# Kernel tuning notes

Measured on AMD Instinct MI355X. Metric: run time of the kernel, lower is better.

The kernel has to match this reference:

```python
import jax, jax.numpy as jnp
import numpy as np
import math

EMBED = 1024
HEADS = 16
HEAD_DIM = EMBED // HEADS
B, S = 2, 2048


def setup_inputs() -> dict:
    key = jax.random.key(0)
    ks = jax.random.split(key, 11)
    s = 1.0 / math.sqrt(EMBED)
    return {
        "query": jax.random.normal(ks[0], (B, S, EMBED), jnp.float32),
        "key_": jax.random.normal(ks[1], (B, S, EMBED), jnp.float32),
        "value": jax.random.normal(ks[2], (B, S, EMBED), jnp.float32),
        "Wq": jax.random.normal(ks[3], (EMBED, EMBED), jnp.float32) * s,
        "bq": jax.random.normal(ks[4], (EMBED,), jnp.float32) * s,
        "Wk": jax.random.normal(ks[5], (EMBED, EMBED), jnp.float32) * s,
        "bk": jax.random.normal(ks[6], (EMBED,), jnp.float32) * s,
        "Wv": jax.random.normal(ks[7], (EMBED, EMBED), jnp.float32) * s,
        "bv": jax.random.normal(ks[8], (EMBED,), jnp.float32) * s,
        "Wo": jax.random.normal(ks[9], (EMBED, EMBED), jnp.float32) * s,
        "bo": jax.random.normal(ks[10], (EMBED,), jnp.float32) * s,
    }


def reference(query, key_, value, Wq, bq, Wk, bk, Wv, bv, Wo, bo):
    b, s, e = query.shape
    # projections (torch Linear: x @ W.T + b)
    q = query @ Wq.T + bq
    k = key_ @ Wk.T + bk
    v = value @ Wv.T + bv
    # [B, H, S, hd]
    q = q.reshape(b, s, HEADS, HEAD_DIM).transpose(0, 2, 1, 3)
    k = k.reshape(b, s, HEADS, HEAD_DIM).transpose(0, 2, 1, 3)
    v = v.reshape(b, s, HEADS, HEAD_DIM).transpose(0, 2, 1, 3)
    scores = jnp.einsum("bhqd,bhkd->bhqk", q, k) / math.sqrt(HEAD_DIM)
    attn = jax.nn.softmax(scores, axis=-1)
    out = jnp.einsum("bhqk,bhkd->bhqd", attn, v)
    out = out.transpose(0, 2, 1, 3).reshape(b, s, e)
    return out @ Wo.T + bo
```

## Files before the change

kernel.cpp:

```cpp
#include <hip/hip_runtime.h>
#include <hip/hip_bf16.h>

using bf16_t = __bf16;
using bf16x4 = __attribute__((ext_vector_type(4))) __bf16;
using bf16x8 = __attribute__((ext_vector_type(8))) __bf16;
using f32x4  = __attribute__((ext_vector_type(4))) float;
using u32 = unsigned int;

constexpr int S_ = 2048, E_ = 1024, M_ = 4096;
constexpr size_t MAT_A = (size_t)M_ * E_;
constexpr size_t MAT_W = (size_t)E_ * E_;

__device__ __forceinline__ bf16_t tobf(float f) {
  unsigned u = __builtin_bit_cast(unsigned, f);
  unsigned short r = (unsigned short)((u + 0x7fffu + ((u >> 16) & 1u)) >> 16);
  return __builtin_bit_cast(bf16_t, r);
}
__device__ __forceinline__ u32 packbf2(float a, float b) {
  u32 ua = __builtin_bit_cast(u32, a) + 0x8000u;
  u32 ub = __builtin_bit_cast(u32, b) + 0x8000u;
  return (ua >> 16) | (ub & 0xffff0000u);
}
__device__ __forceinline__ void async_lds16(const bf16_t* g, bf16_t* l) {
  __builtin_amdgcn_global_load_lds(
      (const __attribute__((address_space(1))) unsigned int*)g,
      (__attribute__((address_space(3))) unsigned int*)l, 16, 0, 0);
}

__global__ __launch_bounds__(256) void cvt7(
    const float* __restrict__ s0, const float* __restrict__ s1,
    const float* __restrict__ s2, const float* __restrict__ s3,
    const float* __restrict__ s4, const float* __restrict__ s5,
    const float* __restrict__ s6,
    bf16_t* __restrict__ d0, bf16_t* __restrict__ d1,
    bf16_t* __restrict__ d2, bf16_t* __restrict__ d3,
    bf16_t* __restrict__ d4, bf16_t* __restrict__ d5,
    bf16_t* __restrict__ d6) {
  const int w = blockIdx.y;
  const size_t n = w < 3 ? MAT_A : MAT_W;
  size_t i = ((size_t)blockIdx.x * 256 + threadIdx.x) * 8;
  if (i >= n) return;
  const float* s = w == 0 ? s0 : w == 1 ? s1 : w == 2 ? s2 : w == 3 ? s3
                 : w == 4 ? s4 : w == 5 ? s5 : s6;
  bf16_t* d = w == 0 ? d0 : w == 1 ? d1 : w == 2 ? d2 : w == 3 ? d3
            : w == 4 ? d4 : w == 5 ? d5 : d6;
  float4 a = *(const float4*)(s + i);
  float4 b = *(const float4*)(s + i + 4);
  bf16x8 o;
  o[0] = tobf(a.x); o[1] = tobf(a.y); o[2] = tobf(a.z); o[3] = tobf(a.w);
  o[4] = tobf(b.x); o[5] = tobf(b.y); o[6] = tobf(b.z); o[7] = tobf(b.w);
  *(bf16x8*)(d + i) = o;
}

__global__ __launch_bounds__(256) void gemm_qkv(
    const bf16_t* __restrict__ xq, const bf16_t* __restrict__ xk,
    const bf16_t* __restrict__ xv, const bf16_t* __restrict__ wq,
    const bf16_t* __restrict__ wk, const bf16_t* __restrict__ wv,
    const float* __restrict__ bq, const float* __restrict__ bk,
    const float* __restrict__ bv, bf16_t* __restrict__ outb,
    bf16_t* __restrict__ Vt) {
  constexpr int K = 1024, N = 1024, BK = 32;
  constexpr float SC = 0.18033688011f;
  __shared__ __align__(16) bf16_t As[128 * BK];
  __shared__ __align__(16) bf16_t Bs[128 * BK];
  const int which = blockIdx.y >> 3;
  const bf16_t* X = which == 0 ? xq : which == 1 ? xk : xv;
  const bf16_t* W = which == 0 ? wq : which == 1 ? wk : wv;
  const float* bias = which == 0 ? bq : which == 1 ? bk : bv;
  const int row0 = blockIdx.x * 128, col0 = (blockIdx.y & 7) * 128;

  const int tid = threadIdx.x, lane = tid & 63, wave = tid >> 6;
  const int l15 = lane & 15, q = lane >> 4;
  const int wm = (wave & 1) * 64, wn = (wave >> 1) * 64;
  const f32x4 fzero = {0.f, 0.f, 0.f, 0.f};

  f32x4 acc[4][4];
#pragma unroll
  for (int i = 0; i < 4; ++i)
#pragma unroll
    for (int j = 0; j < 4; ++j) acc[i][j] = fzero;

  const bf16_t* gA = X + (size_t)(row0 + wave * 32 + (lane >> 2)) * K + (lane & 3) * 8;
  const bf16_t* gB = W + (size_t)(col0 + wave * 32 + (lane >> 2)) * K + (lane & 3) * 8;
  bf16_t* lA = As + wave * 32 * BK;
  bf16_t* lB = Bs + wave * 32 * BK;

  for (int k0 = 0; k0 < K; k0 += BK) {
    __syncthreads();
    async_lds16(gA + k0, lA);
    async_lds16(gA + k0 + 16 * K, lA + 16 * BK);
    async_lds16(gB + k0, lB);
    async_lds16(gB + k0 + 16 * K, lB + 16 * BK);
    __syncthreads();
    bf16x8 af[4], bw[4];
#pragma unroll
    for (int i = 0; i < 4; ++i)
      af[i] = *(const bf16x8*)(As + (wm + i * 16 + l15) * BK + q * 8);
#pragma unroll
    for (int j = 0; j < 4; ++j)
      bw[j] = *(const bf16x8*)(Bs + (wn + j * 16 + l15) * BK + q * 8);
#pragma unroll
    for (int i = 0; i < 4; ++i)
#pragma unroll
      for (int j = 0; j < 4; ++j)
        acc[i][j] = __builtin_amdgcn_mfma_f32_16x16x32_bf16(af[i], bw[j],
                                                            acc[i][j], 0, 0, 0);
  }

  if (which < 2) {
    const float sc = which == 0 ? SC : 1.0f;
    bf16_t* C = outb + (size_t)which * MAT_A;
#pragma unroll
    for (int j = 0; j < 4; ++j) {
      const int col = col0 + wn + j * 16 + l15;
      const float bc = bias[col];
#pragma unroll
      for (int i = 0; i < 4; ++i)
#pragma unroll
        for (int r = 0; r < 4; ++r) {
          const int row = row0 + wm + i * 16 + q * 4 + r;
          C[(size_t)row * N + col] = tobf((acc[i][j][r] + bc) * sc);
        }
    }
  } else {
#pragma unroll
    for (int j = 0; j < 4; ++j) {
      const int col = col0 + wn + j * 16 + l15;
      const float bc = bias[col];
      const int head = col >> 6, d = col & 63;
#pragma unroll
      for (int i = 0; i < 4; ++i) {
        const int row = row0 + wm + i * 16 + q * 4;
        const int bb = row >> 11, tok = row & 2047;
        bf16x4 o;
#pragma unroll
        for (int r = 0; r < 4; ++r) o[r] = tobf(acc[i][j][r] + bc);
        *(bf16x4*)(Vt + ((size_t)(bb * 16 + head) * 64 + d) * S_ + tok) = o;
      }
    }
  }
}

__global__ __launch_bounds__(256) void gemm_o(const bf16_t* __restrict__ X,
                                              const bf16_t* __restrict__ W,
                                              const float* __restrict__ bias,
                                              float* __restrict__ C) {
  constexpr int K = 1024, N = 1024, BK = 32;
  __shared__ __align__(16) bf16_t As[64 * BK];
  __shared__ __align__(16) bf16_t Bs[128 * BK];
  const int tid = threadIdx.x, lane = tid & 63, wave = tid >> 6;
  const int l15 = lane & 15, q = lane >> 4;
  const int row0 = blockIdx.x * 64, col0 = blockIdx.y * 128;
  const int wm = (wave & 1) * 32, wn = (wave >> 1) * 64;
  const f32x4 fzero = {0.f, 0.f, 0.f, 0.f};

  f32x4 acc[2][4];
#pragma unroll
  for (int i = 0; i < 2; ++i)
#pragma unroll
    for (int j = 0; j < 4; ++j) acc[i][j] = fzero;

  const bf16_t* gA = X + (size_t)(row0 + wave * 16 + (lane >> 2)) * K + (lane & 3) * 8;
  const bf16_t* gB = W + (size_t)(col0 + wave * 32 + (lane >> 2)) * K + (lane & 3) * 8;
  bf16_t* lA = As + wave * 16 * BK;
  bf16_t* lB = Bs + wave * 32 * BK;

  for (int k0 = 0; k0 < K; k0 += BK) {
    __syncthreads();
    async_lds16(gA + k0, lA);
    async_lds16(gB + k0, lB);
    async_lds16(gB + k0 + 16 * K, lB + 16 * BK);
    __syncthreads();
    bf16x8 af[2], bw[4];
#pragma unroll
    for (int i = 0; i < 2; ++i)
      af[i] = *(const bf16x8*)(As + (wm + i * 16 + l15) * BK + q * 8);
#pragma unroll
    for (int j = 0; j < 4; ++j)
      bw[j] = *(const bf16x8*)(Bs + (wn + j * 16 + l15) * BK + q * 8);
#pragma unroll
    for (int i = 0; i < 2; ++i)
#pragma unroll
      for (int j = 0; j < 4; ++j)
        acc[i][j] = __builtin_amdgcn_mfma_f32_16x16x32_bf16(af[i], bw[j],
                                                            acc[i][j], 0, 0, 0);
  }

#pragma unroll
  for (int j = 0; j < 4; ++j) {
    const int col = col0 + wn + j * 16 + l15;
    const float bc = bias[col];
#pragma unroll
    for (int i = 0; i < 2; ++i)
#pragma unroll
      for (int r = 0; r < 4; ++r) {
        const int row = row0 + wm + i * 16 + q * 4 + r;
        C[(size_t)row * N + col] = acc[i][j][r] + bc;
      }
  }
}

__global__ __launch_bounds__(256) void attn_mfma(
    const bf16_t* __restrict__ Qm, const bf16_t* __restrict__ Km,
    const bf16_t* __restrict__ Vtg, bf16_t* __restrict__ Om) {
  constexpr int LDP = 72;
  __shared__ __align__(16) bf16_t Ks[2][64 * 64];
  __shared__ __align__(16) bf16_t Vs[2][64 * 64];
  __shared__ __align__(16) bf16_t Ps[4][2][16 * LDP];

  const int tid = threadIdx.x, lane = tid & 63, wave = tid >> 6;
  const int l15 = lane & 15, q = lane >> 4;
  const int bh = blockIdx.x & 31, qb = blockIdx.x >> 5;
  const int b = bh >> 4, h = bh & 15;
  const size_t rowbase = (size_t)b * S_;
  const int hcol = h * 64;
  const int q0 = qb * 128 + wave * 32;

  const int srow = lane >> 3;
  const int schunk = (lane & 7) ^ srow;
  const bf16_t* gK = Km + (rowbase + wave * 16 + srow) * E_ + hcol + schunk * 8;
  const bf16_t* gV = Vtg + ((size_t)bh * 64 + wave * 16 + srow) * S_ + schunk * 8;

  bf16x8 qf[2][2];
#pragma unroll
  for (int qt = 0; qt < 2; ++qt) {
    const bf16_t* qp = Qm + (rowbase + q0 + qt * 16 + l15) * E_ + hcol + q * 8;
    qf[qt][0] = *(const bf16x8*)qp;
    qf[qt][1] = *(const bf16x8*)(qp + 32);
  }

  const f32x4 fzero = {0.f, 0.f, 0.f, 0.f};
  f32x4 oacc[2][4];
#pragma unroll
  for (int qt = 0; qt < 2; ++qt)
#pragma unroll
    for (int mt = 0; mt < 4; ++mt) oacc[qt][mt] = fzero;
  float lsum[2] = {0.f, 0.f};

  const int rbase = l15 * 64;
  int ck[2];
  ck[0] = ((q) ^ (l15 & 7)) * 8;
  ck[1] = ((4 + q) ^ (l15 & 7)) * 8;
  bf16_t* pw0 = Ps[wave][0] + l15 * LDP;
  bf16_t* pw1 = Ps[wave][1] + l15 * LDP;

  async_lds16(gK, Ks[0] + wave * 1024);
  async_lds16(gK + (size_t)8 * E_, Ks[0] + wave * 1024 + 512);
  async_lds16(gV, Vs[0] + wave * 1024);
  async_lds16(gV + (size_t)8 * S_, Vs[0] + wave * 1024 + 512);

  for (int t = 0; t < 32; ++t) {
    const int pb = t & 1;
    __syncthreads();
    if (t + 1 < 32) {
      const size_t koff = (size_t)((t + 1) * 64) * E_;
      const int voff = (t + 1) * 64;
      bf16_t* dK = Ks[pb ^ 1] + wave * 1024;
      bf16_t* dV = Vs[pb ^ 1] + wave * 1024;
      async_lds16(gK + koff, dK);
      async_lds16(gK + koff + (size_t)8 * E_, dK + 512);
      async_lds16(gV + voff, dV);
      async_lds16(gV + voff + (size_t)8 * S_, dV + 512);
    }
    const bf16_t* Kbuf = Ks[pb];
    const bf16_t* Vbuf = Vs[pb];

#pragma unroll
    for (int nt = 0; nt < 4; ++nt) {
      bf16x8 a0 = *(const bf16x8*)(Kbuf + nt * 1024 + rbase + ck[0]);
      bf16x8 a1 = *(const bf16x8*)(Kbuf + nt * 1024 + rbase + ck[1]);
#pragma unroll
      for (int qt = 0; qt < 2; ++qt) {
        f32x4 st = fzero;
        st = __builtin_amdgcn_mfma_f32_16x16x32_bf16(a0, qf[qt][0], st, 0, 0, 0);
        st = __builtin_amdgcn_mfma_f32_16x16x32_bf16(a1, qf[qt][1], st, 0, 0, 0);
        float p0 = __builtin_amdgcn_exp2f(st[0]);
        float p1 = __builtin_amdgcn_exp2f(st[1]);
        float p2 = __builtin_amdgcn_exp2f(st[2]);
        float p3 = __builtin_amdgcn_exp2f(st[3]);
        lsum[qt] += (p0 + p1) + (p2 + p3);
        uint2 pk;
        pk.x = packbf2(p0, p1);
        pk.y = packbf2(p2, p3);
        *(uint2*)((qt ? pw1 : pw0) + nt * 16 + q * 4) = pk;
      }
    }

#pragma unroll
    for (int kk = 0; kk < 2; ++kk) {
      bf16x8 bp0 = *(const bf16x8*)(pw0 + kk * 32 + q * 8);
      bf16x8 bp1 = *(const bf16x8*)(pw1 + kk * 32 + q * 8);
#pragma unroll
      for (int mt = 0; mt < 4; ++mt) {
        bf16x8 av = *(const bf16x8*)(Vbuf + mt * 1024 + rbase + ck[kk]);
        oacc[0][mt] = __builtin_amdgcn_mfma_f32_16x16x32_bf16(av, bp0,
                                                              oacc[0][mt], 0, 0, 0);
        oacc[1][mt] = __builtin_amdgcn_mfma_f32_16x16x32_bf16(av, bp1,
                                                              oacc[1][mt], 0, 0, 0);
      }
    }
  }

#pragma unroll
  for (int qt = 0; qt < 2; ++qt) {
    float l = lsum[qt];
    l += __shfl_xor(l, 16);
    l += __shfl_xor(l, 32);
    const float inv = 1.0f / l;
    const size_t orow = (rowbase + q0 + qt * 16 + l15) * E_ + hcol + q * 4;
#pragma unroll
    for (int mt = 0; mt < 4; ++mt) {
      bf16x4 o;
#pragma unroll
      for (int r = 0; r < 4; ++r) o[r] = tobf(oacc[qt][mt][r] * inv);
      *(bf16x4*)(Om + orow + mt * 16) = o;
    }
  }
}

extern "C" void kernel_launch(void* const* d_in, const int* in_sizes, int n_in,
                              void* d_out, int out_size, void* d_ws, size_t ws_size,
                              hipStream_t stream) {
  const float* query = (const float*)d_in[0];
  const float* key_  = (const float*)d_in[1];
  const float* value = (const float*)d_in[2];
  const float* Wq = (const float*)d_in[3];
  const float* bq = (const float*)d_in[4];
  const float* Wk = (const float*)d_in[5];
  const float* bk = (const float*)d_in[6];
  const float* Wv = (const float*)d_in[7];
  const float* bv = (const float*)d_in[8];
  const float* Wo = (const float*)d_in[9];
  const float* bo = (const float*)d_in[10];

  bf16_t* qc  = (bf16_t*)d_ws;
  bf16_t* kc  = qc + MAT_A;
  bf16_t* vc  = kc + MAT_A;
  bf16_t* wqb = vc + MAT_A;
  bf16_t* wkb = wqb + MAT_W;
  bf16_t* wvb = wkb + MAT_W;
  bf16_t* wob = wvb + MAT_W;
  bf16_t* Qb  = wob + MAT_W;
  bf16_t* Kb  = Qb + MAT_A;
  bf16_t* Vt  = Kb + MAT_A;
  bf16_t* AOb = Vt + MAT_A;

  cvt7<<<dim3(MAT_A / 2048, 7), 256, 0, stream>>>(
      query, key_, value, Wq, Wk, Wv, Wo,
      qc, kc, vc, wqb, wkb, wvb, wob);
  gemm_qkv<<<dim3(32, 24), 256, 0, stream>>>(qc, kc, vc, wqb, wkb, wvb,
                                             bq, bk, bv, Qb, Vt);
  attn_mfma<<<512, 256, 0, stream>>>(Qb, Kb, Vt, AOb);
  gemm_o<<<dim3(64, 8), 256, 0, stream>>>(AOb, wob, bo, (float*)d_out);
}
```

Before: 238.9 us.

## Load K/V fragments directly from global and compute row sums via MFMA

Removes the LDS double-buffered async staging of K and V tiles and the per-iteration block barrier, so each wave loads its MFMA operand fragments straight from global memory (relying on L1/L2 for reuse across waves). The softmax denominator is now computed with an extra MFMA against a ones vector on the bf16-rounded probabilities, instead of scalar adds plus cross-lane shuffles. The cost is four times more global/L2 traffic for K and V per block, and load latency exposed without explicit prefetch.

```diff
diff --git a/kernel.cpp b/kernel.cpp
--- a/kernel.cpp
+++ b/kernel.cpp
@@ -204,8 +204,6 @@
     const bf16_t* __restrict__ Qm, const bf16_t* __restrict__ Km,
     const bf16_t* __restrict__ Vtg, bf16_t* __restrict__ Om) {
   constexpr int LDP = 72;
-  __shared__ __align__(16) bf16_t Ks[2][64 * 64];
-  __shared__ __align__(16) bf16_t Vs[2][64 * 64];
   __shared__ __align__(16) bf16_t Ps[4][2][16 * LDP];
 
   const int tid = threadIdx.x, lane = tid & 63, wave = tid >> 6;
@@ -216,11 +214,6 @@
   const int hcol = h * 64;
   const int q0 = qb * 128 + wave * 32;
 
-  const int srow = lane >> 3;
-  const int schunk = (lane & 7) ^ srow;
-  const bf16_t* gK = Km + (rowbase + wave * 16 + srow) * E_ + hcol + schunk * 8;
-  const bf16_t* gV = Vtg + ((size_t)bh * 64 + wave * 16 + srow) * S_ + schunk * 8;
-
   bf16x8 qf[2][2];
 #pragma unroll
   for (int qt = 0; qt < 2; ++qt) {
@@ -229,56 +222,44 @@
     qf[qt][1] = *(const bf16x8*)(qp + 32);
   }
 
+  bf16x8 onesv;
+#pragma unroll
+  for (int j = 0; j < 8; ++j)
+    onesv[j] = __builtin_bit_cast(bf16_t, (unsigned short)0x3F80);
+
   const f32x4 fzero = {0.f, 0.f, 0.f, 0.f};
   f32x4 oacc[2][4];
 #pragma unroll
   for (int qt = 0; qt < 2; ++qt)
 #pragma unroll
     for (int mt = 0; mt < 4; ++mt) oacc[qt][mt] = fzero;
-  float lsum[2] = {0.f, 0.f};
-
-  const int rbase = l15 * 64;
-  int ck[2];
-  ck[0] = ((q) ^ (l15 & 7)) * 8;
-  ck[1] = ((4 + q) ^ (l15 & 7)) * 8;
+  f32x4 lsacc[2] = {fzero, fzero};
+
+  const bf16_t* Kb = Km + (rowbase + l15) * E_ + hcol + q * 8;
+  const bf16_t* Vb = Vtg + ((size_t)bh * 64 + l15) * S_ + q * 8;
   bf16_t* pw0 = Ps[wave][0] + l15 * LDP;
   bf16_t* pw1 = Ps[wave][1] + l15 * LDP;
 
-  async_lds16(gK, Ks[0] + wave * 1024);
-  async_lds16(gK + (size_t)8 * E_, Ks[0] + wave * 1024 + 512);
-  async_lds16(gV, Vs[0] + wave * 1024);
-  async_lds16(gV + (size_t)8 * S_, Vs[0] + wave * 1024 + 512);
-
-  for (int t = 0; t < 32; ++t) {
-    const int pb = t & 1;
-    __syncthreads();
-    if (t + 1 < 32) {
-      const size_t koff = (size_t)((t + 1) * 64) * E_;
-      const int voff = (t + 1) * 64;
-      bf16_t* dK = Ks[pb ^ 1] + wave * 1024;
-      bf16_t* dV = Vs[pb ^ 1] + wave * 1024;
-      async_lds16(gK + koff, dK);
-      async_lds16(gK + koff + (size_t)8 * E_, dK + 512);
-      async_lds16(gV + voff, dV);
-      async_lds16(gV + voff + (size_t)8 * S_, dV + 512);
-    }
-    const bf16_t* Kbuf = Ks[pb];
-    const bf16_t* Vbuf = Vs[pb];
-
+  for (int kt = 0; kt < S_; kt += 64) {
+    bf16x8 kf[4][2];
 #pragma unroll
     for (int nt = 0; nt < 4; ++nt) {
-      bf16x8 a0 = *(const bf16x8*)(Kbuf + nt * 1024 + rbase + ck[0]);
-      bf16x8 a1 = *(const bf16x8*)(Kbuf + nt * 1024 + rbase + ck[1]);
+      const bf16_t* kp = Kb + (size_t)(kt + nt * 16) * E_;
+      kf[nt][0] = *(const bf16x8*)kp;
+      kf[nt][1] = *(const bf16x8*)(kp + 32);
+    }
+
+#pragma unroll
+    for (int nt = 0; nt < 4; ++nt) {
 #pragma unroll
       for (int qt = 0; qt < 2; ++qt) {
         f32x4 st = fzero;
-        st = __builtin_amdgcn_mfma_f32_16x16x32_bf16(a0, qf[qt][0], st, 0, 0, 0);
-        st = __builtin_amdgcn_mfma_f32_16x16x32_bf16(a1, qf[qt][1], st, 0, 0, 0);
+        st = __builtin_amdgcn_mfma_f32_16x16x32_bf16(kf[nt][0], qf[qt][0], st, 0, 0, 0);
+        st = __builtin_amdgcn_mfma_f32_16x16x32_bf16(kf[nt][1], qf[qt][1], st, 0, 0, 0);
         float p0 = __builtin_amdgcn_exp2f(st[0]);
         float p1 = __builtin_amdgcn_exp2f(st[1]);
         float p2 = __builtin_amdgcn_exp2f(st[2]);
         float p3 = __builtin_amdgcn_exp2f(st[3]);
-        lsum[qt] += (p0 + p1) + (p2 + p3);
         uint2 pk;
         pk.x = packbf2(p0, p1);
         pk.y = packbf2(p2, p3);
@@ -290,9 +271,11 @@
     for (int kk = 0; kk < 2; ++kk) {
       bf16x8 bp0 = *(const bf16x8*)(pw0 + kk * 32 + q * 8);
       bf16x8 bp1 = *(const bf16x8*)(pw1 + kk * 32 + q * 8);
+      lsacc[0] = __builtin_amdgcn_mfma_f32_16x16x32_bf16(onesv, bp0, lsacc[0], 0, 0, 0);
+      lsacc[1] = __builtin_amdgcn_mfma_f32_16x16x32_bf16(onesv, bp1, lsacc[1], 0, 0, 0);
 #pragma unroll
       for (int mt = 0; mt < 4; ++mt) {
-        bf16x8 av = *(const bf16x8*)(Vbuf + mt * 1024 + rbase + ck[kk]);
+        bf16x8 av = *(const bf16x8*)(Vb + (size_t)(mt * 16) * S_ + kt + kk * 32);
         oacc[0][mt] = __builtin_amdgcn_mfma_f32_16x16x32_bf16(av, bp0,
                                                               oacc[0][mt], 0, 0, 0);
         oacc[1][mt] = __builtin_amdgcn_mfma_f32_16x16x32_bf16(av, bp1,
@@ -303,10 +286,7 @@
 
 #pragma unroll
   for (int qt = 0; qt < 2; ++qt) {
-    float l = lsum[qt];
-    l += __shfl_xor(l, 16);
-    l += __shfl_xor(l, 32);
-    const float inv = 1.0f / l;
+    const float inv = 1.0f / lsacc[qt][0];
     const size_t orow = (rowbase + q0 + qt * 16 + l15) * E_ + hcol + q * 4;
 #pragma unroll
     for (int mt = 0; mt < 4; ++mt) {
```

Result: slower. 300.5 us (+25.8%).
